# Kernel tuning notes

Measured on AMD Instinct MI355X. Metric: run time of the kernel, lower is better.

The kernel has to match this reference:

```python
import jax, jax.numpy as jnp
import numpy as np

D = 128
LN_EPS = 1e-5

def _mlp2(x, W1, b1, W2, b2):
    return jax.nn.silu(x @ W1 + b1) @ W2 + b2

def setup_inputs() -> dict:
    key = jax.random.key(0)
    ks = jax.random.split(key, 20)
    B, N = 2, 512
    inp = {
        'scalar_features': jax.random.normal(ks[0], (B, N, D), jnp.float32),
        'vector_features': jax.random.normal(ks[1], (B, N, 3), jnp.float32),
        'positions': jax.random.normal(ks[2], (B, N, 3), jnp.float32),
        'pair_mask': jnp.ones((B, N, N), jnp.float32),
        'conservation': jax.random.uniform(ks[3], (B, N, 1), jnp.float32),
    }
    s = 0.02
    inp['eW1'] = jax.random.normal(ks[4], (2 * D + 4, D), jnp.float32) * s
    inp['eb1'] = jnp.zeros((D,), jnp.float32)
    inp['eW2'] = jax.random.normal(ks[5], (D, D), jnp.float32) * s
    inp['eb2'] = jnp.zeros((D,), jnp.float32)
    inp['sW1'] = jax.random.normal(ks[6], (2 * D, D), jnp.float32) * s
    inp['sb1'] = jnp.zeros((D,), jnp.float32)
    inp['sW2'] = jax.random.normal(ks[7], (D, D), jnp.float32) * s
    inp['sb2'] = jnp.zeros((D,), jnp.float32)
    inp['vW1'] = jax.random.normal(ks[8], (D, D), jnp.float32) * s
    inp['vb1'] = jnp.zeros((D,), jnp.float32)
    inp['vW2'] = jax.random.normal(ks[9], (D, 1), jnp.float32) * s
    inp['vb2'] = jnp.zeros((1,), jnp.float32)
    inp['ln_w'] = jnp.ones((D,), jnp.float32)
    inp['ln_b'] = jnp.zeros((D,), jnp.float32)
    return inp

def reference(scalar_features, vector_features, positions, pair_mask, conservation,
              eW1, eb1, eW2, eb2, sW1, sb1, sW2, sb2, vW1, vb1, vW2, vb2, ln_w, ln_b):
    N = scalar_features.shape[-2]
    # rel[b,i,j] = pos[b,i] - pos[b,j]
    rel = positions[..., :, None, :] - positions[..., None, :, :]          # [B,N,N,3]
    dist = jnp.maximum(jnp.linalg.norm(rel, axis=-1, keepdims=True), 1e-8)  # [B,N,N,1]
    direction = rel / dist
    feat_i = jnp.broadcast_to(scalar_features[..., :, None, :], scalar_features.shape[:-2] + (N, N, D))
    feat_j = jnp.broadcast_to(scalar_features[..., None, :, :], scalar_features.shape[:-2] + (N, N, D))
    cons_i = jnp.broadcast_to(conservation[..., :, None, :], conservation.shape[:-2] + (N, N, 1))
    cons_j = jnp.broadcast_to(conservation[..., None, :, :], conservation.shape[:-2] + (N, N, 1))
    edge_input = jnp.concatenate([feat_i, feat_j, dist, cons_i, cons_j, pair_mask[..., None]], axis=-1)
    edge_hidden = _mlp2(edge_input, eW1, eb1, eW2, eb2)                    # [B,N,N,D]
    edge_weights = jax.nn.sigmoid(edge_hidden.mean(axis=-1)) * pair_mask   # [B,N,N]
    message_scalar = (edge_hidden * edge_weights[..., None]).sum(axis=-2)  # sum over j -> [B,N,D]
    upd = _mlp2(jnp.concatenate([scalar_features, message_scalar], axis=-1), sW1, sb1, sW2, sb2)
    x = scalar_features + upd
    mu = x.mean(axis=-1, keepdims=True)
    var = x.var(axis=-1, keepdims=True)
    scalar_out = (x - mu) * jax.lax.rsqrt(var + LN_EPS) * ln_w + ln_b
    vector_gate = _mlp2(edge_hidden, vW1, vb1, vW2, vb2)[..., 0] * edge_weights  # [B,N,N]
    vector_message = (vector_gate[..., None] * direction).sum(axis=-2)           # [B,N,3]
    vector_out = vector_features + vector_message
    return scalar_out, vector_out, edge_weights
```

## Files before the change

### kernel.cpp

```cpp
#include <hip/hip_runtime.h>

#define DD 128
#define NN 512
#define NODES 1024
#define TILE 64

typedef short bf16x8 __attribute__((ext_vector_type(8)));
typedef float f32x4 __attribute__((ext_vector_type(4)));

__device__ __forceinline__ float sigmoidf_(float x) {
  return __builtin_amdgcn_rcpf(1.f + __expf(-x));
}
__device__ __forceinline__ float siluf_(float x) { return x * sigmoidf_(x); }

__device__ __forceinline__ unsigned short f2bf_(float v) {
  unsigned int u = __float_as_uint(v);
  u += 0x7fffu + ((u >> 16) & 1u);
  return (unsigned short)(u >> 16);
}
__device__ __forceinline__ unsigned cvtpk_(float lo, float hi) {
  unsigned r;
  asm("v_cvt_pk_bf16_f32 %0, %1, %2" : "=v"(r) : "v"(lo), "v"(hi));
  return r;
}
__device__ __forceinline__ float bflo_(unsigned u) { return __uint_as_float(u << 16); }
__device__ __forceinline__ float bfhi_(unsigned u) { return __uint_as_float(u & 0xffff0000u); }

__global__ __launch_bounds__(128) void prep_kernel(
    const float* __restrict__ sf, const float* __restrict__ cons,
    const float* __restrict__ eW1, const float* __restrict__ eb1,
    const float* __restrict__ eW2, const float* __restrict__ eb2,
    const float* __restrict__ vW1, const float* __restrict__ vb1,
    float* __restrict__ Ag, float* __restrict__ Bvg,
    unsigned short* __restrict__ E2V1T, float* __restrict__ m2,
    float* __restrict__ c1, float* __restrict__ mb)
{
  const int bid = blockIdx.x;
  const int d = threadIdx.x;
  if (bid < NODES) {
    float c = cons[bid];
    float aacc = c * eW1[258*DD + d];
    float bacc = eb1[d] + c * eW1[257*DD + d];
    const float* sfrow = sf + bid*DD;
    #pragma unroll 4
    for (int k = 0; k < DD; ++k) {
      float s = sfrow[k];
      aacc = fmaf(s, eW1[(128+k)*DD + d], aacc);
      bacc = fmaf(s, eW1[k*DD + d], bacc);
    }
    Ag[bid*DD + d]  = aacc;
    Bvg[bid*DD + d] = bacc;
  } else if (bid < NODES + 128) {
    const int k = bid - NODES;
    float acc = 0.f;
    #pragma unroll 4
    for (int t = 0; t < DD; ++t) acc = fmaf(eW2[k*DD + t], vW1[t*DD + d], acc);
    E2V1T[d*DD + k] = f2bf_(acc);
    if (d == 0) {
      float s = 0.f;
      for (int t = 0; t < DD; ++t) s += eW2[k*DD + t];
      m2[k] = s * (1.0f/128.0f);
    }
  } else {
    float acc = vb1[d];
    #pragma unroll 4
    for (int k = 0; k < DD; ++k) acc = fmaf(eb2[k], vW1[k*DD + d], acc);
    c1[d] = acc;
    if (d == 0) {
      float s = 0.f;
      for (int k = 0; k < DD; ++k) s += eb2[k];
      mb[0] = s * (1.0f/128.0f);
    }
  }
}

__global__ __launch_bounds__(256, 4) void edge_kernel(
    const float* __restrict__ sf, const float* __restrict__ vf,
    const float* __restrict__ pos, const float* __restrict__ pm,
    const float* __restrict__ eW1,
    const float* __restrict__ eW2, const float* __restrict__ eb2,
    const float* __restrict__ sW1, const float* __restrict__ sb1,
    const float* __restrict__ sW2, const float* __restrict__ sb2,
    const float* __restrict__ vW2g, const float* __restrict__ vb2g,
    const float* __restrict__ lnw, const float* __restrict__ lnb,
    const float* __restrict__ Ag, const float* __restrict__ Bvg,
    const unsigned short* __restrict__ E2V1Tg, const float* __restrict__ m2g,
    const float* __restrict__ c1g, const float* __restrict__ mbg,
    float* __restrict__ sout, float* __restrict__ vout, float* __restrict__ ewout)
{
  __shared__ __align__(16) unsigned short hbf[TILE*128];
  __shared__ __align__(16) float BvL[DD], w256L[DD], w259L[DD], m2L[DD];
  __shared__ float distA[NN], maskA[NN], wA[NN];
  __shared__ float dirA[NN][3];
  __shared__ float gpart[4][TILE];
  __shared__ float redS[4], redA[2], redB[2];

  const int tid = threadIdx.x;
  const int ni  = blockIdx.x;
  const int nb  = ni & ~(NN - 1);

  const int l   = tid & 63, w = tid >> 6;
  const int l15 = l & 15,  lg = l >> 4;
  const int d   = tid & 127, sub = tid >> 7;
  const int g16 = tid >> 4, db = (tid & 15) * 8;

  if (tid < 128) {
    BvL[tid]   = Bvg[(size_t)ni*DD + tid];
    w256L[tid] = eW1[256*DD + tid];
    w259L[tid] = eW1[259*DD + tid];
    m2L[tid]   = m2g[tid];
  }
  {
    float pix = pos[ni*3+0], piy = pos[ni*3+1], piz = pos[ni*3+2];
    #pragma unroll
    for (int rep = 0; rep < 2; ++rep) {
      int j = tid + rep*256;
      float rx = pix - pos[(nb + j)*3 + 0];
      float ry = piy - pos[(nb + j)*3 + 1];
      float rz = piz - pos[(nb + j)*3 + 2];
      float dist = fmaxf(sqrtf(rx*rx + ry*ry + rz*rz), 1e-8f);
      distA[j] = dist;
      float inv = __builtin_amdgcn_rcpf(dist);
      dirA[j][0] = rx*inv; dirA[j][1] = ry*inv; dirA[j][2] = rz*inv;
      maskA[j] = pm[(size_t)ni*NN + j];
    }
  }

  float c1r2[2], vw2r2[2];
  #pragma unroll
  for (int ct = 0; ct < 2; ++ct) {
    int dc = w*32 + ct*16 + l15;
    c1r2[ct] = c1g[dc]; vw2r2[ct] = vW2g[dc];
  }
  const float mbv = mbg[0], vb2v = vb2g[0];

  float Sreg8[8];
  #pragma unroll
  for (int m = 0; m < 8; ++m) Sreg8[m] = 0.f;
  float vmx = 0.f, vmy = 0.f, vmz = 0.f;

  for (int tile = 0; tile < 8; ++tile) {
    const int jt0 = tile * TILE;
    __syncthreads();
    {
      float4 bv0 = *(const float4*)&BvL[db],   bv1 = *(const float4*)&BvL[db+4];
      float4 wa0 = *(const float4*)&w256L[db], wa1 = *(const float4*)&w256L[db+4];
      float4 wb0 = *(const float4*)&w259L[db], wb1 = *(const float4*)&w259L[db+4];
      float4 m20 = *(const float4*)&m2L[db],   m21 = *(const float4*)&m2L[db+4];
      #pragma unroll
      for (int it = 0; it < 4; ++it) {
        int j = it*16 + g16;
        int jj = jt0 + j;
        const float4* ag = (const float4*)&Ag[(size_t)(nb + jj)*DD + db];
        float4 a0 = ag[0], a1 = ag[1];
        float dj = distA[jj], mj = maskA[jj];
        float h0 = siluf_(bv0.x + a0.x + dj*wa0.x + mj*wb0.x);
        float h1 = siluf_(bv0.y + a0.y + dj*wa0.y + mj*wb0.y);
        float h2 = siluf_(bv0.z + a0.z + dj*wa0.z + mj*wb0.z);
        float h3 = siluf_(bv0.w + a0.w + dj*wa0.w + mj*wb0.w);
        float h4 = siluf_(bv1.x + a1.x + dj*wa1.x + mj*wb1.x);
        float h5 = siluf_(bv1.y + a1.y + dj*wa1.y + mj*wb1.y);
        float h6 = siluf_(bv1.z + a1.z + dj*wa1.z + mj*wb1.z);
        float h7 = siluf_(bv1.w + a1.w + dj*wa1.w + mj*wb1.w);
        uint4 pk;
        pk.x = cvtpk_(h0, h1); pk.y = cvtpk_(h2, h3);
        pk.z = cvtpk_(h4, h5); pk.w = cvtpk_(h6, h7);
        *(uint4*)&hbf[j*128 + (db ^ ((j & 7) << 3))] = pk;
        float psum = h0*m20.x + h1*m20.y + h2*m20.z + h3*m20.w
                   + h4*m21.x + h5*m21.y + h6*m21.z + h7*m21.w;
        psum += __shfl_xor(psum, 1);
        psum += __shfl_xor(psum, 2);
        psum += __shfl_xor(psum, 4);
        psum += __shfl_xor(psum, 8);
        if ((tid & 15) == 0) {
          float w_ = mj * sigmoidf_(psum + mbv);
          wA[jj] = w_;
          ewout[(size_t)ni*NN + jj] = w_;
        }
      }
    }
    __syncthreads();
    {
      f32x4 cfr[4][2];
      #pragma unroll
      for (int mt = 0; mt < 4; ++mt) {
        cfr[mt][0] = (f32x4){0.f,0.f,0.f,0.f};
        cfr[mt][1] = (f32x4){0.f,0.f,0.f,0.f};
      }
      #pragma unroll
      for (int kk = 0; kk < 4; ++kk) {
        const int kb = kk*32 + lg*8;
        bf16x8 bf0 = *(const bf16x8*)&E2V1Tg[(size_t)(w*32 + l15)*128 + kb];
        bf16x8 bf1 = *(const bf16x8*)&E2V1Tg[(size_t)(w*32 + 16 + l15)*128 + kb];
        #pragma unroll
        for (int mt = 0; mt < 4; ++mt) {
          int row = mt*16 + l15;
          bf16x8 af = *(const bf16x8*)&hbf[row*128 + (kb ^ ((row & 7) << 3))];
          cfr[mt][0] = __builtin_amdgcn_mfma_f32_16x16x32_bf16(af, bf0, cfr[mt][0], 0, 0, 0);
          cfr[mt][1] = __builtin_amdgcn_mfma_f32_16x16x32_bf16(af, bf1, cfr[mt][1], 0, 0, 0);
        }
      }
      #pragma unroll
      for (int mt = 0; mt < 4; ++mt) {
        #pragma unroll
        for (int r = 0; r < 4; ++r) {
          float v0 = siluf_(cfr[mt][0][r] + c1r2[0]) * vw2r2[0]
                   + siluf_(cfr[mt][1][r] + c1r2[1]) * vw2r2[1];
          v0 += __shfl_xor(v0, 1);
          v0 += __shfl_xor(v0, 2);
          v0 += __shfl_xor(v0, 4);
          v0 += __shfl_xor(v0, 8);
          if (l15 == 0) gpart[w][mt*16 + lg*4 + r] = v0;
        }
      }
    }
    __syncthreads();
    if (w == 0) {
      int j = l;
      float g = (gpart[0][j] + gpart[1][j] + gpart[2][j] + gpart[3][j] + vb2v) * wA[jt0 + j];
      vmx = fmaf(g, dirA[jt0 + j][0], vmx);
      vmy = fmaf(g, dirA[jt0 + j][1], vmy);
      vmz = fmaf(g, dirA[jt0 + j][2], vmz);
    }
    #pragma unroll
    for (int r = 0; r < 4; ++r) {
      int j = g16*4 + r;
      float wj = wA[jt0 + j];
      uint4 hv = *(const uint4*)&hbf[j*128 + (db ^ ((j & 7) << 3))];
      Sreg8[0] = fmaf(wj, bflo_(hv.x), Sreg8[0]);
      Sreg8[1] = fmaf(wj, bfhi_(hv.x), Sreg8[1]);
      Sreg8[2] = fmaf(wj, bflo_(hv.y), Sreg8[2]);
      Sreg8[3] = fmaf(wj, bfhi_(hv.y), Sreg8[3]);
      Sreg8[4] = fmaf(wj, bflo_(hv.z), Sreg8[4]);
      Sreg8[5] = fmaf(wj, bfhi_(hv.z), Sreg8[5]);
      Sreg8[6] = fmaf(wj, bflo_(hv.w), Sreg8[6]);
      Sreg8[7] = fmaf(wj, bfhi_(hv.w), Sreg8[7]);
    }
  }

  float* scr   = (float*)hbf;
  float* Spart = scr;
  float* SL    = scr + 512;
  float* partA = scr + 640;
  float* msgL  = scr + 768;
  float* u1L   = scr + 896;
  float* xoL   = scr + 1024;

  __syncthreads();
  #pragma unroll
  for (int m = 0; m < 8; ++m) {
    float s = Sreg8[m];
    s += __shfl_xor(s, 16);
    s += __shfl_xor(s, 32);
    if (l < 16) Spart[w*128 + l*8 + m] = s;
  }
  {
    float sw = wA[tid] + wA[tid + 256];
    #pragma unroll
    for (int off = 1; off < 64; off <<= 1) sw += __shfl_xor(sw, off);
    if (l == 0) redS[w] = sw;
  }
  if (w == 0) {
    #pragma unroll
    for (int off = 1; off < 64; off <<= 1) {
      vmx += __shfl_xor(vmx, off);
      vmy += __shfl_xor(vmy, off);
      vmz += __shfl_xor(vmz, off);
    }
    if (l == 0) {
      vout[ni*3 + 0] = vf[ni*3 + 0] + vmx;
      vout[ni*3 + 1] = vf[ni*3 + 1] + vmy;
      vout[ni*3 + 2] = vf[ni*3 + 2] + vmz;
    }
  }
  __syncthreads();
  if (tid < 128) SL[tid] = Spart[tid] + Spart[128 + tid] + Spart[256 + tid] + Spart[384 + tid];
  __syncthreads();
  const float sumwv = redS[0] + redS[1] + redS[2] + redS[3];

  float p = 0.f;
  { int k0 = sub*64;
    #pragma unroll 4
    for (int k = k0; k < k0 + 64; ++k) p = fmaf(SL[k], eW2[k*DD + d], p); }
  if (sub) partA[d] = p;
  __syncthreads();
  if (!sub) msgL[d] = p + partA[d] + sumwv * eb2[d];
  __syncthreads();

  float q = 0.f;
  if (!sub) {
    const float* xr = sf + (size_t)ni*DD;
    #pragma unroll 4
    for (int t = 0; t < 128; ++t) q = fmaf(xr[t], sW1[t*DD + d], q);
  } else {
    #pragma unroll 4
    for (int t = 0; t < 128; ++t) q = fmaf(msgL[t], sW1[(128 + t)*DD + d], q);
  }
  if (sub) partA[d] = q;
  __syncthreads();
  if (!sub) u1L[d] = siluf_(q + partA[d] + sb1[d]);
  __syncthreads();

  float r2 = 0.f;
  { int t0 = sub*64;
    #pragma unroll 4
    for (int t = t0; t < t0 + 64; ++t) r2 = fmaf(u1L[t], sW2[t*DD + d], r2); }
  if (sub) partA[d] = r2;
  __syncthreads();
  if (!sub) xoL[d] = sf[(size_t)ni*DD + d] + r2 + partA[d] + sb2[d];
  __syncthreads();

  if (tid < 128) {
    float v = xoL[tid];
    float s1 = v, s2 = v*v;
    #pragma unroll
    for (int off = 1; off < 64; off <<= 1) { s1 += __shfl_xor(s1, off); s2 += __shfl_xor(s2, off); }
    if ((tid & 63) == 0) { redA[tid >> 6] = s1; redB[tid >> 6] = s2; }
  }
  __syncthreads();
  if (tid < 128) {
    float s1 = redA[0] + redA[1], s2 = redB[0] + redB[1];
    float mu = s1 * 0.0078125f;
    float var = s2 * 0.0078125f - mu*mu;
    sout[(size_t)ni*DD + tid] = (xoL[tid] - mu) * rsqrtf(var + 1e-5f) * lnw[tid] + lnb[tid];
  }
}

extern "C" void kernel_launch(void* const* d_in, const int* in_sizes, int n_in,
                              void* d_out, int out_size, void* d_ws, size_t ws_size,
                              hipStream_t stream) {
  const float* sf   = (const float*)d_in[0];
  const float* vf   = (const float*)d_in[1];
  const float* pos  = (const float*)d_in[2];
  const float* pm   = (const float*)d_in[3];
  const float* cons = (const float*)d_in[4];
  const float* eW1  = (const float*)d_in[5];
  const float* eb1  = (const float*)d_in[6];
  const float* eW2  = (const float*)d_in[7];
  const float* eb2  = (const float*)d_in[8];
  const float* sW1  = (const float*)d_in[9];
  const float* sb1  = (const float*)d_in[10];
  const float* sW2  = (const float*)d_in[11];
  const float* sb2  = (const float*)d_in[12];
  const float* vW1  = (const float*)d_in[13];
  const float* vb1  = (const float*)d_in[14];
  const float* vW2  = (const float*)d_in[15];
  const float* vb2  = (const float*)d_in[16];
  const float* lnw  = (const float*)d_in[17];
  const float* lnb  = (const float*)d_in[18];

  float* ws   = (float*)d_ws;
  float* Ag   = ws;
  float* Bvg  = ws + 131072;
  float* m2   = ws + 262144;
  float* c1   = ws + 262272;
  float* mb   = ws + 262400;
  unsigned short* E2V1T = (unsigned short*)(ws + 262404);

  float* sout  = (float*)d_out;
  float* vout  = sout + 131072;
  float* ewout = sout + 134144;

  hipLaunchKernelGGL(prep_kernel, dim3(NODES + 129), dim3(128), 0, stream,
                     sf, cons, eW1, eb1, eW2, eb2, vW1, vb1,
                     Ag, Bvg, E2V1T, m2, c1, mb);
  hipLaunchKernelGGL(edge_kernel, dim3(NODES), dim3(256), 0, stream,
                     sf, vf, pos, pm, eW1, eW2, eb2, sW1, sb1, sW2, sb2,
                     vW2, vb2, lnw, lnb, Ag, Bvg, E2V1T, m2, c1, mb,
                     sout, vout, ewout);
}
```

Before: 101.3 us.

## Build MFMA A-fragments in registers and cache swizzled weight matrix in LDS

The edge loop is restructured so that each wave computes its 16 edge rows of silu hidden activations directly into MFMA A-operand registers, instead of staging a 64-row tile in shared memory behind block-wide barriers. The full bf16 E2V1T matrix (32 KB, stored pre-swizzled by the prep kernel) is copied into LDS once per block and used as the B operand for all 8 column tiles. Edge weights, weighted message sums and vector-gate contributions are all reduced with wave shuffles, which removes the per-tile __syncthreads and the dist/dir/mask/weight LDS arrays. In exchange, register pressure rises (32-entry S accumulator, 8 column constants) and each block first loads 32 KB of LDS, which may reduce occupancy.

```diff
diff --git a/kernel.cpp b/kernel.cpp
--- a/kernel.cpp
+++ b/kernel.cpp
@@ -3,7 +3,6 @@
 #define DD 128
 #define NN 512
 #define NODES 1024
-#define TILE 64
 
 typedef short bf16x8 __attribute__((ext_vector_type(8)));
 typedef float f32x4 __attribute__((ext_vector_type(4)));
@@ -55,7 +54,7 @@
     float acc = 0.f;
     #pragma unroll 4
     for (int t = 0; t < DD; ++t) acc = fmaf(eW2[k*DD + t], vW1[t*DD + d], acc);
-    E2V1T[d*DD + k] = f2bf_(acc);
+    E2V1T[d*DD + (k ^ ((d & 7) << 3))] = f2bf_(acc);
     if (d == 0) {
       float s = 0.f;
       for (int t = 0; t < DD; ++t) s += eW2[k*DD + t];
@@ -88,12 +87,9 @@
     const float* __restrict__ c1g, const float* __restrict__ mbg,
     float* __restrict__ sout, float* __restrict__ vout, float* __restrict__ ewout)
 {
-  __shared__ __align__(16) unsigned short hbf[TILE*128];
+  __shared__ __align__(16) unsigned short eTs[128*128];
   __shared__ __align__(16) float BvL[DD], w256L[DD], w259L[DD], m2L[DD];
-  __shared__ float distA[NN], maskA[NN], wA[NN];
-  __shared__ float dirA[NN][3];
-  __shared__ float gpart[4][TILE];
-  __shared__ float redS[4], redA[2], redB[2];
+  __shared__ float redS[4], redVx[4], redVy[4], redVz[4], redA[2], redB[2];
 
   const int tid = threadIdx.x;
   const int ni  = blockIdx.x;
@@ -102,143 +98,137 @@
   const int l   = tid & 63, w = tid >> 6;
   const int l15 = l & 15,  lg = l >> 4;
   const int d   = tid & 127, sub = tid >> 7;
-  const int g16 = tid >> 4, db = (tid & 15) * 8;
-
+  const int d0base = lg*8;
+
+  {
+    const uint4* src = (const uint4*)E2V1Tg;
+    uint4* dst = (uint4*)eTs;
+    #pragma unroll
+    for (int it = 0; it < 8; ++it) dst[tid + it*256] = src[tid + it*256];
+  }
   if (tid < 128) {
     BvL[tid]   = Bvg[(size_t)ni*DD + tid];
     w256L[tid] = eW1[256*DD + tid];
     w259L[tid] = eW1[259*DD + tid];
     m2L[tid]   = m2g[tid];
   }
-  {
-    float pix = pos[ni*3+0], piy = pos[ni*3+1], piz = pos[ni*3+2];
-    #pragma unroll
-    for (int rep = 0; rep < 2; ++rep) {
-      int j = tid + rep*256;
-      float rx = pix - pos[(nb + j)*3 + 0];
-      float ry = piy - pos[(nb + j)*3 + 1];
-      float rz = piz - pos[(nb + j)*3 + 2];
-      float dist = fmaxf(sqrtf(rx*rx + ry*ry + rz*rz), 1e-8f);
-      distA[j] = dist;
-      float inv = __builtin_amdgcn_rcpf(dist);
-      dirA[j][0] = rx*inv; dirA[j][1] = ry*inv; dirA[j][2] = rz*inv;
-      maskA[j] = pm[(size_t)ni*NN + j];
-    }
-  }
-
-  float c1r2[2], vw2r2[2];
+  const float pix = pos[ni*3+0], piy = pos[ni*3+1], piz = pos[ni*3+2];
+  float c1r[8], vw2r[8];
   #pragma unroll
-  for (int ct = 0; ct < 2; ++ct) {
-    int dc = w*32 + ct*16 + l15;
-    c1r2[ct] = c1g[dc]; vw2r2[ct] = vW2g[dc];
+  for (int ct = 0; ct < 8; ++ct) {
+    int col = ct*16 + l15;
+    c1r[ct] = c1g[col]; vw2r[ct] = vW2g[col];
   }
   const float mbv = mbg[0], vb2v = vb2g[0];
 
-  float Sreg8[8];
+  float Sreg[4][8];
   #pragma unroll
-  for (int m = 0; m < 8; ++m) Sreg8[m] = 0.f;
-  float vmx = 0.f, vmy = 0.f, vmz = 0.f;
-
-  for (int tile = 0; tile < 8; ++tile) {
-    const int jt0 = tile * TILE;
-    __syncthreads();
-    {
-      float4 bv0 = *(const float4*)&BvL[db],   bv1 = *(const float4*)&BvL[db+4];
-      float4 wa0 = *(const float4*)&w256L[db], wa1 = *(const float4*)&w256L[db+4];
-      float4 wb0 = *(const float4*)&w259L[db], wb1 = *(const float4*)&w259L[db+4];
-      float4 m20 = *(const float4*)&m2L[db],   m21 = *(const float4*)&m2L[db+4];
-      #pragma unroll
-      for (int it = 0; it < 4; ++it) {
-        int j = it*16 + g16;
-        int jj = jt0 + j;
-        const float4* ag = (const float4*)&Ag[(size_t)(nb + jj)*DD + db];
-        float4 a0 = ag[0], a1 = ag[1];
-        float dj = distA[jj], mj = maskA[jj];
-        float h0 = siluf_(bv0.x + a0.x + dj*wa0.x + mj*wb0.x);
-        float h1 = siluf_(bv0.y + a0.y + dj*wa0.y + mj*wb0.y);
-        float h2 = siluf_(bv0.z + a0.z + dj*wa0.z + mj*wb0.z);
-        float h3 = siluf_(bv0.w + a0.w + dj*wa0.w + mj*wb0.w);
-        float h4 = siluf_(bv1.x + a1.x + dj*wa1.x + mj*wb1.x);
-        float h5 = siluf_(bv1.y + a1.y + dj*wa1.y + mj*wb1.y);
-        float h6 = siluf_(bv1.z + a1.z + dj*wa1.z + mj*wb1.z);
-        float h7 = siluf_(bv1.w + a1.w + dj*wa1.w + mj*wb1.w);
-        uint4 pk;
-        pk.x = cvtpk_(h0, h1); pk.y = cvtpk_(h2, h3);
-        pk.z = cvtpk_(h4, h5); pk.w = cvtpk_(h6, h7);
-        *(uint4*)&hbf[j*128 + (db ^ ((j & 7) << 3))] = pk;
-        float psum = h0*m20.x + h1*m20.y + h2*m20.z + h3*m20.w
-                   + h4*m21.x + h5*m21.y + h6*m21.z + h7*m21.w;
-        psum += __shfl_xor(psum, 1);
-        psum += __shfl_xor(psum, 2);
-        psum += __shfl_xor(psum, 4);
-        psum += __shfl_xor(psum, 8);
-        if ((tid & 15) == 0) {
-          float w_ = mj * sigmoidf_(psum + mbv);
-          wA[jj] = w_;
-          ewout[(size_t)ni*NN + jj] = w_;
-        }
+  for (int kk = 0; kk < 4; ++kk)
+    #pragma unroll
+    for (int m = 0; m < 8; ++m) Sreg[kk][m] = 0.f;
+  float vmx = 0.f, vmy = 0.f, vmz = 0.f, swacc = 0.f;
+
+  __syncthreads();
+
+  for (int t = 0; t < 8; ++t) {
+    const int row = t*64 + w*16 + l15;
+    float px = pos[(nb + row)*3 + 0];
+    float py = pos[(nb + row)*3 + 1];
+    float pz = pos[(nb + row)*3 + 2];
+    float rx = pix - px, ry = piy - py, rz = piz - pz;
+    float dist = fmaxf(sqrtf(rx*rx + ry*ry + rz*rz), 1e-8f);
+    float inv = __builtin_amdgcn_rcpf(dist);
+    float dirx = rx*inv, diry = ry*inv, dirz = rz*inv;
+    float mj = pm[(size_t)ni*NN + row];
+
+    union { uint4 u; bf16x8 b; } af[4];
+    float dot = 0.f;
+    const float* agrow = Ag + (size_t)(nb + row)*DD;
+    #pragma unroll
+    for (int kk = 0; kk < 4; ++kk) {
+      const int d0 = kk*32 + d0base;
+      float4 a0 = *(const float4*)(agrow + d0), a1 = *(const float4*)(agrow + d0 + 4);
+      float4 b0 = *(const float4*)&BvL[d0],   b1 = *(const float4*)&BvL[d0+4];
+      float4 wa0= *(const float4*)&w256L[d0], wa1= *(const float4*)&w256L[d0+4];
+      float4 wb0= *(const float4*)&w259L[d0], wb1= *(const float4*)&w259L[d0+4];
+      float4 m20= *(const float4*)&m2L[d0],   m21= *(const float4*)&m2L[d0+4];
+      float h0 = siluf_(b0.x + a0.x + dist*wa0.x + mj*wb0.x);
+      float h1 = siluf_(b0.y + a0.y + dist*wa0.y + mj*wb0.y);
+      float h2 = siluf_(b0.z + a0.z + dist*wa0.z + mj*wb0.z);
+      float h3 = siluf_(b0.w + a0.w + dist*wa0.w + mj*wb0.w);
+      float h4 = siluf_(b1.x + a1.x + dist*wa1.x + mj*wb1.x);
+      float h5 = siluf_(b1.y + a1.y + dist*wa1.y + mj*wb1.y);
+      float h6 = siluf_(b1.z + a1.z + dist*wa1.z + mj*wb1.z);
+      float h7 = siluf_(b1.w + a1.w + dist*wa1.w + mj*wb1.w);
+      af[kk].u.x = cvtpk_(h0, h1);
+      af[kk].u.y = cvtpk_(h2, h3);
+      af[kk].u.z = cvtpk_(h4, h5);
+      af[kk].u.w = cvtpk_(h6, h7);
+      dot += h0*m20.x + h1*m20.y + h2*m20.z + h3*m20.w
+           + h4*m21.x + h5*m21.y + h6*m21.z + h7*m21.w;
+    }
+    dot += __shfl_xor(dot, 16);
+    dot += __shfl_xor(dot, 32);
+    const float w_full = mj * sigmoidf_(dot + mbv);
+    if (l < 16) {
+      ewout[(size_t)ni*NN + row] = w_full;
+      swacc += w_full;
+    }
+    #pragma unroll
+    for (int kk = 0; kk < 4; ++kk) {
+      Sreg[kk][0] = fmaf(w_full, bflo_(af[kk].u.x), Sreg[kk][0]);
+      Sreg[kk][1] = fmaf(w_full, bfhi_(af[kk].u.x), Sreg[kk][1]);
+      Sreg[kk][2] = fmaf(w_full, bflo_(af[kk].u.y), Sreg[kk][2]);
+      Sreg[kk][3] = fmaf(w_full, bfhi_(af[kk].u.y), Sreg[kk][3]);
+      Sreg[kk][4] = fmaf(w_full, bflo_(af[kk].u.z), Sreg[kk][4]);
+      Sreg[kk][5] = fmaf(w_full, bfhi_(af[kk].u.z), Sreg[kk][5]);
+      Sreg[kk][6] = fmaf(w_full, bflo_(af[kk].u.w), Sreg[kk][6]);
+      Sreg[kk][7] = fmaf(w_full, bfhi_(af[kk].u.w), Sreg[kk][7]);
+    }
+
+    float gp[4] = {0.f, 0.f, 0.f, 0.f};
+    #pragma unroll
+    for (int ct = 0; ct < 8; ++ct) {
+      const int col = ct*16 + l15;
+      const int swz = (col & 7) << 3;
+      const unsigned short* ecol = &eTs[col*DD];
+      bf16x8 bf0 = *(const bf16x8*)&ecol[(  0 + d0base) ^ swz];
+      bf16x8 bf1 = *(const bf16x8*)&ecol[( 32 + d0base) ^ swz];
+      bf16x8 bf2 = *(const bf16x8*)&ecol[( 64 + d0base) ^ swz];
+      bf16x8 bf3 = *(const bf16x8*)&ecol[( 96 + d0base) ^ swz];
+      f32x4 c = {0.f, 0.f, 0.f, 0.f};
+      c = __builtin_amdgcn_mfma_f32_16x16x32_bf16(af[0].b, bf0, c, 0, 0, 0);
+      c = __builtin_amdgcn_mfma_f32_16x16x32_bf16(af[1].b, bf1, c, 0, 0, 0);
+      c = __builtin_amdgcn_mfma_f32_16x16x32_bf16(af[2].b, bf2, c, 0, 0, 0);
+      c = __builtin_amdgcn_mfma_f32_16x16x32_bf16(af[3].b, bf3, c, 0, 0, 0);
+      gp[0] += siluf_(c[0] + c1r[ct]) * vw2r[ct];
+      gp[1] += siluf_(c[1] + c1r[ct]) * vw2r[ct];
+      gp[2] += siluf_(c[2] + c1r[ct]) * vw2r[ct];
+      gp[3] += siluf_(c[3] + c1r[ct]) * vw2r[ct];
+    }
+    #pragma unroll
+    for (int r = 0; r < 4; ++r) {
+      float v = gp[r];
+      v += __shfl_xor(v, 1);
+      v += __shfl_xor(v, 2);
+      v += __shfl_xor(v, 4);
+      v += __shfl_xor(v, 8);
+      const int srow = lg*4 + r;
+      float wrow = __shfl(w_full, srow);
+      float g = (v + vb2v) * wrow;
+      float dx = __shfl(dirx, srow);
+      float dy = __shfl(diry, srow);
+      float dz = __shfl(dirz, srow);
+      if (l15 == 0) {
+        vmx = fmaf(g, dx, vmx);
+        vmy = fmaf(g, dy, vmy);
+        vmz = fmaf(g, dz, vmz);
       }
     }
-    __syncthreads();
-    {
-      f32x4 cfr[4][2];
-      #pragma unroll
-      for (int mt = 0; mt < 4; ++mt) {
-        cfr[mt][0] = (f32x4){0.f,0.f,0.f,0.f};
-        cfr[mt][1] = (f32x4){0.f,0.f,0.f,0.f};
-      }
-      #pragma unroll
-      for (int kk = 0; kk < 4; ++kk) {
-        const int kb = kk*32 + lg*8;
-        bf16x8 bf0 = *(const bf16x8*)&E2V1Tg[(size_t)(w*32 + l15)*128 + kb];
-        bf16x8 bf1 = *(const bf16x8*)&E2V1Tg[(size_t)(w*32 + 16 + l15)*128 + kb];
-        #pragma unroll
-        for (int mt = 0; mt < 4; ++mt) {
-          int row = mt*16 + l15;
-          bf16x8 af = *(const bf16x8*)&hbf[row*128 + (kb ^ ((row & 7) << 3))];
-          cfr[mt][0] = __builtin_amdgcn_mfma_f32_16x16x32_bf16(af, bf0, cfr[mt][0], 0, 0, 0);
-          cfr[mt][1] = __builtin_amdgcn_mfma_f32_16x16x32_bf16(af, bf1, cfr[mt][1], 0, 0, 0);
-        }
-      }
-      #pragma unroll
-      for (int mt = 0; mt < 4; ++mt) {
-        #pragma unroll
-        for (int r = 0; r < 4; ++r) {
-          float v0 = siluf_(cfr[mt][0][r] + c1r2[0]) * vw2r2[0]
-                   + siluf_(cfr[mt][1][r] + c1r2[1]) * vw2r2[1];
-          v0 += __shfl_xor(v0, 1);
-          v0 += __shfl_xor(v0, 2);
-          v0 += __shfl_xor(v0, 4);
-          v0 += __shfl_xor(v0, 8);
-          if (l15 == 0) gpart[w][mt*16 + lg*4 + r] = v0;
-        }
-      }
-    }
-    __syncthreads();
-    if (w == 0) {
-      int j = l;
-      float g = (gpart[0][j] + gpart[1][j] + gpart[2][j] + gpart[3][j] + vb2v) * wA[jt0 + j];
-      vmx = fmaf(g, dirA[jt0 + j][0], vmx);
-      vmy = fmaf(g, dirA[jt0 + j][1], vmy);
-      vmz = fmaf(g, dirA[jt0 + j][2], vmz);
-    }
-    #pragma unroll
-    for (int r = 0; r < 4; ++r) {
-      int j = g16*4 + r;
-      float wj = wA[jt0 + j];
-      uint4 hv = *(const uint4*)&hbf[j*128 + (db ^ ((j & 7) << 3))];
-      Sreg8[0] = fmaf(wj, bflo_(hv.x), Sreg8[0]);
-      Sreg8[1] = fmaf(wj, bfhi_(hv.x), Sreg8[1]);
-      Sreg8[2] = fmaf(wj, bflo_(hv.y), Sreg8[2]);
-      Sreg8[3] = fmaf(wj, bfhi_(hv.y), Sreg8[3]);
-      Sreg8[4] = fmaf(wj, bflo_(hv.z), Sreg8[4]);
-      Sreg8[5] = fmaf(wj, bfhi_(hv.z), Sreg8[5]);
-      Sreg8[6] = fmaf(wj, bflo_(hv.w), Sreg8[6]);
-      Sreg8[7] = fmaf(wj, bfhi_(hv.w), Sreg8[7]);
-    }
-  }
-
-  float* scr   = (float*)hbf;
+  }
+
+  __syncthreads();
+  float* scr   = (float*)eTs;
   float* Spart = scr;
   float* SL    = scr + 512;
   float* partA = scr + 640;
@@ -246,35 +236,47 @@
   float* u1L   = scr + 896;
   float* xoL   = scr + 1024;
 
-  __syncthreads();
   #pragma unroll
-  for (int m = 0; m < 8; ++m) {
-    float s = Sreg8[m];
-    s += __shfl_xor(s, 16);
-    s += __shfl_xor(s, 32);
-    if (l < 16) Spart[w*128 + l*8 + m] = s;
+  for (int kk = 0; kk < 4; ++kk)
+    #pragma unroll
+    for (int m = 0; m < 8; ++m) {
+      float v = Sreg[kk][m];
+      v += __shfl_xor(v, 1);
+      v += __shfl_xor(v, 2);
+      v += __shfl_xor(v, 4);
+      v += __shfl_xor(v, 8);
+      Sreg[kk][m] = v;
+    }
+  if (l15 == 0) {
+    #pragma unroll
+    for (int kk = 0; kk < 4; ++kk)
+      #pragma unroll
+      for (int m = 0; m < 8; ++m)
+        Spart[w*128 + kk*32 + lg*8 + m] = Sreg[kk][m];
   }
   {
-    float sw = wA[tid] + wA[tid + 256];
+    float sw = swacc;
     #pragma unroll
     for (int off = 1; off < 64; off <<= 1) sw += __shfl_xor(sw, off);
     if (l == 0) redS[w] = sw;
   }
-  if (w == 0) {
+  {
+    float vx = vmx, vy = vmy, vz = vmz;
     #pragma unroll
     for (int off = 1; off < 64; off <<= 1) {
-      vmx += __shfl_xor(vmx, off);
-      vmy += __shfl_xor(vmy, off);
-      vmz += __shfl_xor(vmz, off);
-    }
-    if (l == 0) {
-      vout[ni*3 + 0] = vf[ni*3 + 0] + vmx;
-      vout[ni*3 + 1] = vf[ni*3 + 1] + vmy;
-      vout[ni*3 + 2] = vf[ni*3 + 2] + vmz;
-    }
-  }
-  __syncthreads();
-  if (tid < 128) SL[tid] = Spart[tid] + Spart[128 + tid] + Spart[256 + tid] + Spart[384 + tid];
+      vx += __shfl_xor(vx, off);
+      vy += __shfl_xor(vy, off);
+      vz += __shfl_xor(vz, off);
+    }
+    if (l == 0) { redVx[w] = vx; redVy[w] = vy; redVz[w] = vz; }
+  }
+  __syncthreads();
+  if (tid < 128) SL[tid] = Spart[tid] + Spart[128+tid] + Spart[256+tid] + Spart[384+tid];
+  if (tid == 0) {
+    vout[ni*3 + 0] = vf[ni*3 + 0] + redVx[0]+redVx[1]+redVx[2]+redVx[3];
+    vout[ni*3 + 1] = vf[ni*3 + 1] + redVy[0]+redVy[1]+redVy[2]+redVy[3];
+    vout[ni*3 + 2] = vf[ni*3 + 2] + redVz[0]+redVz[1]+redVz[2]+redVz[3];
+  }
   __syncthreads();
   const float sumwv = redS[0] + redS[1] + redS[2] + redS[3];
 
@@ -291,10 +293,10 @@
   if (!sub) {
     const float* xr = sf + (size_t)ni*DD;
     #pragma unroll 4
-    for (int t = 0; t < 128; ++t) q = fmaf(xr[t], sW1[t*DD + d], q);
+    for (int tt = 0; tt < 128; ++tt) q = fmaf(xr[tt], sW1[tt*DD + d], q);
   } else {
     #pragma unroll 4
-    for (int t = 0; t < 128; ++t) q = fmaf(msgL[t], sW1[(128 + t)*DD + d], q);
+    for (int tt = 0; tt < 128; ++tt) q = fmaf(msgL[tt], sW1[(128 + tt)*DD + d], q);
   }
   if (sub) partA[d] = q;
   __syncthreads();
@@ -304,7 +306,7 @@
   float r2 = 0.f;
   { int t0 = sub*64;
     #pragma unroll 4
-    for (int t = t0; t < t0 + 64; ++t) r2 = fmaf(u1L[t], sW2[t*DD + d], r2); }
+    for (int tt = t0; tt < t0 + 64; ++tt) r2 = fmaf(u1L[tt], sW2[tt*DD + d], r2); }
   if (sub) partA[d] = r2;
   __syncthreads();
   if (!sub) xoL[d] = sf[(size_t)ni*DD + d] + r2 + partA[d] + sb2[d];
```

Result: slower. 111.6 us (+10.2%).
